# Kernel tuning notes

Hardware: AMD Instinct MI355X
Metric: run time of the kernel (lower is better)

The kernel has to match this reference:

```python
import jax, jax.numpy as jnp
import numpy as np

R = 65536          # number of RoI proposals
D = 1024           # pooled feature dim (input_shape.channels)
C = 20             # num_classes (num_classes_stuff == 2 -> heads output num_classes)


def setup_inputs() -> dict:
    key = jax.random.key(0)
    k1, k2, k3 = jax.random.split(key, 3)
    x = jax.random.normal(k1, (R, D), dtype=jnp.float32)
    # xavier_uniform init for the two heads
    lim = float(np.sqrt(6.0 / (D + C)))
    W_cls = jax.random.uniform(k2, (C, D), dtype=jnp.float32, minval=-lim, maxval=lim)
    W_det = jax.random.uniform(k3, (C, D), dtype=jnp.float32, minval=-lim, maxval=lim)
    b_cls = jnp.zeros((C,), dtype=jnp.float32)
    b_det = jnp.zeros((C,), dtype=jnp.float32)
    return {"x": x, "W_cls": W_cls, "b_cls": b_cls, "W_det": W_det, "b_det": b_det}


def reference(x, W_cls, b_cls, W_det, b_det):
    # Flatten features if needed (torch.flatten(x, start_dim=1))
    x = x.reshape(x.shape[0], -1)
    cls_logits = x @ W_cls.T + b_cls          # [R, C]
    det_logits = x @ W_det.T + b_det          # [R, C]
    # WSDDN/JTSM MIL head: softmax over classes x softmax over proposals
    pred_cls = jax.nn.softmax(cls_logits, axis=1)
    pred_det = jax.nn.softmax(det_logits, axis=0)
    scores = pred_cls * pred_det              # [R, C] per-proposal per-class scores
    return scores
```

## Files before the change

### kernel.cpp

```cpp
#include <hip/hip_runtime.h>
#include <math.h>

#define NROWS 65536
#define NDIM  1024
#define NCLS  20

__global__ __launch_bounds__(256) void repack_w_k(
    const float* __restrict__ Wc, const float* __restrict__ Wd,
    float* __restrict__ Wt, float* __restrict__ colsum)
{
    int i = blockIdx.x * 256 + threadIdx.x;
    int d = i / 40;
    int c = i % 40;
    float v = (c < NCLS) ? Wc[c * NDIM + d] : Wd[(c - NCLS) * NDIM + d];
    Wt[i] = v;
    if (i < NCLS) colsum[i] = 0.0f;
}

__global__ __launch_bounds__(256, 2) void main_gemm_k(
    const float* __restrict__ x,   const float* __restrict__ Wt,
    const float* __restrict__ bc,  const float* __restrict__ bd,
    float* __restrict__ out,       float* __restrict__ colsum)
{
    const int tid  = threadIdx.x;
    const int wave = tid >> 6;
    const int lane = tid & 63;
    const int pair = wave >> 1;
    const int h    = wave & 1;
    const int hu   = __builtin_amdgcn_readfirstlane(h);

    const int row = blockIdx.x * 128 + pair * 64 + lane;
    const float* __restrict__ xr    = x  + (size_t)row * NDIM;
    const float* __restrict__ wbase = Wt + hu * NCLS;

    float acc[NCLS];
#pragma unroll
    for (int c = 0; c < NCLS; ++c) acc[c] = 0.0f;

    float4 buf[4];
#pragma unroll
    for (int i = 0; i < 4; ++i) buf[i] = ((const float4*)xr)[i];

    for (int d0 = 0; d0 < NDIM; d0 += 16) {
        float4 cur[4];
#pragma unroll
        for (int i = 0; i < 4; ++i) cur[i] = buf[i];
        if (d0 + 16 < NDIM) {
#pragma unroll
            for (int i = 0; i < 4; ++i)
                buf[i] = ((const float4*)(xr + d0 + 16))[i];
        }
        const float* __restrict__ wch = wbase + d0 * 40;
#pragma unroll
        for (int dd = 0; dd < 16; ++dd) {
            const float xs = ((const float*)cur)[dd];
            const float* __restrict__ wd = wch + dd * 40;
#pragma unroll
            for (int c = 0; c < NCLS; ++c)
                acc[c] = fmaf(xs, wd[c], acc[c]);
        }
    }

    __shared__ float e_det[2][64][NCLS];

    if (h == 1) {
        float e[NCLS];
#pragma unroll
        for (int c = 0; c < NCLS; ++c) e[c] = expf(acc[c] + bd[c]);
#pragma unroll
        for (int c = 0; c < NCLS; ++c) {
            float v = e[c];
            v += __shfl_xor(v, 32, 64);
            v += __shfl_xor(v, 16, 64);
            v += __shfl_xor(v,  8, 64);
            v += __shfl_xor(v,  4, 64);
            v += __shfl_xor(v,  2, 64);
            v += __shfl_xor(v,  1, 64);
            if (lane == 0) atomicAdd(&colsum[c], v);
        }
#pragma unroll
        for (int c = 0; c < NCLS; ++c) e_det[pair][lane][c] = e[c];
    }
    __syncthreads();
    if (h == 0) {
        float l2[NCLS];
        float m = -3.402823466e+38f;
#pragma unroll
        for (int c = 0; c < NCLS; ++c) { l2[c] = acc[c] + bc[c]; m = fmaxf(m, l2[c]); }
        float e[NCLS], s = 0.0f;
#pragma unroll
        for (int c = 0; c < NCLS; ++c) { e[c] = expf(l2[c] - m); s += e[c]; }
        const float inv = 1.0f / s;
        float ov[NCLS];
#pragma unroll
        for (int c = 0; c < NCLS; ++c)
            ov[c] = e[c] * inv * e_det[pair][lane][c];
        float* __restrict__ orow = out + (size_t)row * NCLS;
#pragma unroll
        for (int i = 0; i < 5; ++i)
            ((float4*)orow)[i] = make_float4(ov[4*i], ov[4*i+1], ov[4*i+2], ov[4*i+3]);
    }
}

__global__ void finalize_k(const float* __restrict__ colsum, float* __restrict__ inv)
{
    int c = threadIdx.x;
    if (c < NCLS) inv[c] = 1.0f / colsum[c];
}

__global__ __launch_bounds__(256) void scale_k(
    float* __restrict__ out, const float* __restrict__ inv)
{
    int i = blockIdx.x * 256 + threadIdx.x;
    int base = (i * 4) % NCLS;
    float4 v = ((float4*)out)[i];
    v.x *= inv[base + 0];
    v.y *= inv[base + 1];
    v.z *= inv[base + 2];
    v.w *= inv[base + 3];
    ((float4*)out)[i] = v;
}

extern "C" void kernel_launch(void* const* d_in, const int* in_sizes, int n_in,
                              void* d_out, int out_size, void* d_ws, size_t ws_size,
                              hipStream_t stream)
{
    const float* x  = (const float*)d_in[0];
    const float* Wc = (const float*)d_in[1];
    const float* bc = (const float*)d_in[2];
    const float* Wd = (const float*)d_in[3];
    const float* bd = (const float*)d_in[4];
    float* out = (float*)d_out;

    float* Wt     = (float*)d_ws;
    float* colsum = Wt + NDIM * 2 * NCLS;
    float* inv    = colsum + NCLS;

    repack_w_k<<<(NDIM * 2 * NCLS) / 256, 256, 0, stream>>>(Wc, Wd, Wt, colsum);
    main_gemm_k<<<NROWS / 128, 256, 0, stream>>>(x, Wt, bc, bd, out, colsum);
    finalize_k<<<1, 64, 0, stream>>>(colsum, inv);
    scale_k<<<(NROWS * NCLS / 4) / 256, 256, 0, stream>>>(out, inv);
}
```

Measured before the change: 656.6 us.

## Split GEMM K dimension across 8 waves with shared-memory tree reduction

Each 512-thread block now handles 64 rows, and each of its 8 waves computes all 40 outputs (cls and det) over a 128-wide slice of the feature dimension. The partial sums are combined through a shared-memory tree reduction, after which wave 0 does both softmaxes and writes the output. Previously two waves each read the full x row for 20 classes, so x was loaded twice. The new layout reads each x element once and raises occupancy, at the cost of 40 accumulators per thread, LDS reduction traffic, and several block barriers.

```diff
diff --git a/kernel.cpp b/kernel.cpp
--- a/kernel.cpp
+++ b/kernel.cpp
@@ -4,72 +4,96 @@
 #define NROWS 65536
 #define NDIM  1024
 #define NCLS  20
+#define NOUT  40
+#define KSEG  8
+#define KLEN  128
 
 __global__ __launch_bounds__(256) void repack_w_k(
     const float* __restrict__ Wc, const float* __restrict__ Wd,
     float* __restrict__ Wt, float* __restrict__ colsum)
 {
     int i = blockIdx.x * 256 + threadIdx.x;
-    int d = i / 40;
-    int c = i % 40;
+    int d = i / NOUT;
+    int c = i % NOUT;
     float v = (c < NCLS) ? Wc[c * NDIM + d] : Wd[(c - NCLS) * NDIM + d];
     Wt[i] = v;
     if (i < NCLS) colsum[i] = 0.0f;
 }
 
-__global__ __launch_bounds__(256, 2) void main_gemm_k(
+__global__ __launch_bounds__(512, 8) void main_gemm_k(
     const float* __restrict__ x,   const float* __restrict__ Wt,
     const float* __restrict__ bc,  const float* __restrict__ bd,
     float* __restrict__ out,       float* __restrict__ colsum)
 {
     const int tid  = threadIdx.x;
-    const int wave = tid >> 6;
     const int lane = tid & 63;
-    const int pair = wave >> 1;
-    const int h    = wave & 1;
-    const int hu   = __builtin_amdgcn_readfirstlane(h);
+    const int w    = tid >> 6;
+    const int wu   = __builtin_amdgcn_readfirstlane(w);
+    const int row  = blockIdx.x * 64 + lane;
 
-    const int row = blockIdx.x * 128 + pair * 64 + lane;
-    const float* __restrict__ xr    = x  + (size_t)row * NDIM;
-    const float* __restrict__ wbase = Wt + hu * NCLS;
+    const float* __restrict__ xr   = x  + (size_t)row * NDIM + wu * KLEN;
+    const float* __restrict__ wseg = Wt + wu * KLEN * NOUT;
 
-    float acc[NCLS];
+    float acc[NOUT];
 #pragma unroll
-    for (int c = 0; c < NCLS; ++c) acc[c] = 0.0f;
+    for (int c = 0; c < NOUT; ++c) acc[c] = 0.0f;
 
-    float4 buf[4];
+    for (int d0 = 0; d0 < KLEN; d0 += 8) {
+        float4 c0 = ((const float4*)(xr + d0))[0];
+        float4 c1 = ((const float4*)(xr + d0))[1];
+        float cur[8];
+        *(float4*)(cur + 0) = c0;
+        *(float4*)(cur + 4) = c1;
+        const float* __restrict__ wch = wseg + d0 * NOUT;
 #pragma unroll
-    for (int i = 0; i < 4; ++i) buf[i] = ((const float4*)xr)[i];
-
-    for (int d0 = 0; d0 < NDIM; d0 += 16) {
-        float4 cur[4];
+        for (int dd = 0; dd < 8; ++dd) {
+            const float xs = cur[dd];
 #pragma unroll
-        for (int i = 0; i < 4; ++i) cur[i] = buf[i];
-        if (d0 + 16 < NDIM) {
-#pragma unroll
-            for (int i = 0; i < 4; ++i)
-                buf[i] = ((const float4*)(xr + d0 + 16))[i];
-        }
-        const float* __restrict__ wch = wbase + d0 * 40;
-#pragma unroll
-        for (int dd = 0; dd < 16; ++dd) {
-            const float xs = ((const float*)cur)[dd];
-            const float* __restrict__ wd = wch + dd * 40;
-#pragma unroll
-            for (int c = 0; c < NCLS; ++c)
-                acc[c] = fmaf(xs, wd[c], acc[c]);
+            for (int c = 0; c < NOUT; ++c)
+                acc[c] = fmaf(xs, wch[dd * NOUT + c], acc[c]);
         }
     }
 
-    __shared__ float e_det[2][64][NCLS];
+    __shared__ float red[NOUT][256];
 
-    if (h == 1) {
-        float e[NCLS];
+    if (w >= 4) {
+        const int s = tid - 256;
 #pragma unroll
-        for (int c = 0; c < NCLS; ++c) e[c] = expf(acc[c] + bd[c]);
+        for (int c = 0; c < NOUT; ++c) red[c][s] = acc[c];
+    }
+    __syncthreads();
+    if (w < 4) {
+#pragma unroll
+        for (int c = 0; c < NOUT; ++c) acc[c] += red[c][tid];
+    }
+    __syncthreads();
+    if (w == 2 || w == 3) {
+        const int s = tid - 128;
+#pragma unroll
+        for (int c = 0; c < NOUT; ++c) red[c][s] = acc[c];
+    }
+    __syncthreads();
+    if (w < 2) {
+#pragma unroll
+        for (int c = 0; c < NOUT; ++c) acc[c] += red[c][tid];
+    }
+    __syncthreads();
+    if (w == 1) {
+#pragma unroll
+        for (int c = 0; c < NOUT; ++c) red[c][tid - 64] = acc[c];
+    }
+    __syncthreads();
+
+    if (w == 0) {
+#pragma unroll
+        for (int c = 0; c < NOUT; ++c) acc[c] += red[c][lane];
+
+#pragma unroll
+        for (int c = 0; c < NCLS; ++c) acc[NCLS + c] = expf(acc[NCLS + c] + bd[c]);
+
 #pragma unroll
         for (int c = 0; c < NCLS; ++c) {
-            float v = e[c];
+            float v = acc[NCLS + c];
             v += __shfl_xor(v, 32, 64);
             v += __shfl_xor(v, 16, 64);
             v += __shfl_xor(v,  8, 64);
@@ -78,27 +102,25 @@
             v += __shfl_xor(v,  1, 64);
             if (lane == 0) atomicAdd(&colsum[c], v);
         }
-#pragma unroll
-        for (int c = 0; c < NCLS; ++c) e_det[pair][lane][c] = e[c];
-    }
-    __syncthreads();
-    if (h == 0) {
-        float l2[NCLS];
+
         float m = -3.402823466e+38f;
 #pragma unroll
-        for (int c = 0; c < NCLS; ++c) { l2[c] = acc[c] + bc[c]; m = fmaxf(m, l2[c]); }
-        float e[NCLS], s = 0.0f;
+        for (int c = 0; c < NCLS; ++c) { acc[c] += bc[c]; m = fmaxf(m, acc[c]); }
+        float s = 0.0f;
 #pragma unroll
-        for (int c = 0; c < NCLS; ++c) { e[c] = expf(l2[c] - m); s += e[c]; }
+        for (int c = 0; c < NCLS; ++c) { acc[c] = expf(acc[c] - m); s += acc[c]; }
         const float inv = 1.0f / s;
-        float ov[NCLS];
-#pragma unroll
-        for (int c = 0; c < NCLS; ++c)
-            ov[c] = e[c] * inv * e_det[pair][lane][c];
+
         float* __restrict__ orow = out + (size_t)row * NCLS;
 #pragma unroll
-        for (int i = 0; i < 5; ++i)
-            ((float4*)orow)[i] = make_float4(ov[4*i], ov[4*i+1], ov[4*i+2], ov[4*i+3]);
+        for (int i = 0; i < 5; ++i) {
+            float4 v;
+            v.x = acc[4*i + 0] * inv * acc[NCLS + 4*i + 0];
+            v.y = acc[4*i + 1] * inv * acc[NCLS + 4*i + 1];
+            v.z = acc[4*i + 2] * inv * acc[NCLS + 4*i + 2];
+            v.w = acc[4*i + 3] * inv * acc[NCLS + 4*i + 3];
+            ((float4*)orow)[i] = v;
+        }
     }
 }
 
@@ -133,11 +155,11 @@
     float* out = (float*)d_out;
 
     float* Wt     = (float*)d_ws;
-    float* colsum = Wt + NDIM * 2 * NCLS;
+    float* colsum = Wt + NDIM * NOUT;
     float* inv    = colsum + NCLS;
 
-    repack_w_k<<<(NDIM * 2 * NCLS) / 256, 256, 0, stream>>>(Wc, Wd, Wt, colsum);
-    main_gemm_k<<<NROWS / 128, 256, 0, stream>>>(x, Wt, bc, bd, out, colsum);
+    repack_w_k<<<(NDIM * NOUT) / 256, 256, 0, stream>>>(Wc, Wd, Wt, colsum);
+    main_gemm_k<<<NROWS / 64, 512, 0, stream>>>(x, Wt, bc, bd, out, colsum);
     finalize_k<<<1, 64, 0, stream>>>(colsum, inv);
     scale_k<<<(NROWS * NCLS / 4) / 256, 256, 0, stream>>>(out, inv);
 }
```

Result: faster. 598.7 us (-8.8%).
